# Optimization experiments

Hardware: AMD Instinct MI355X
Metric: run time of the kernel (lower is better)

Reference implementation:

```python
import jax, jax.numpy as jnp
import numpy as np

NUM_TABLES = 10
EMB_DIM = 3
VOCAB = 1_000_000
N_IDX = 4_000_000
N_BAGS = 100_000


def setup_inputs() -> dict:
    key = jax.random.key(0)
    k_idx, k_off, k_w = jax.random.split(key, 3)
    eb_input = jax.random.randint(k_idx, (N_IDX,), 0, VOCAB, dtype=jnp.int64)
    # EmbeddingBag offsets: sorted, first element must be 0, values in [0, N_IDX)
    eb_offset = jnp.sort(jax.random.randint(k_off, (N_BAGS,), 0, N_IDX, dtype=jnp.int64))
    eb_offset = eb_offset.at[0].set(0)
    # torch.nn.EmbeddingBag default init: N(0, 1)
    W = jax.random.normal(k_w, (NUM_TABLES, VOCAB, EMB_DIM), dtype=jnp.float32)
    return {"eb_input": eb_input, "eb_offset": eb_offset, "W": W}


def _bag_sums(eb_input, eb_offset, W):
    # segment id for each index position: bag b covers [offset[b], offset[b+1])
    n = eb_input.shape[0]
    seg = jnp.searchsorted(eb_offset, jnp.arange(n), side="right") - 1  # [N]
    gathered = W[:, eb_input, :]  # [T, N, D] irregular gather
    # sum-pool per bag for every table
    per_bag = jax.vmap(lambda g: jax.ops.segment_sum(g, seg, num_segments=eb_offset.shape[0]))(gathered)  # [T, B, D]
    return per_bag


def reference(eb_input, eb_offset, W):
    per_bag = _bag_sums(eb_input, eb_offset, W)  # [10, B, 3]
    outs = [per_bag[i] for i in range(NUM_TABLES)]
    outs[5] = jnp.sum(outs[5], axis=1, keepdims=True)  # [B, 1]
    outs[6] = jnp.sum(outs[6], axis=1, keepdims=True)  # [B, 1]
    cat = jnp.concatenate(outs, axis=1)  # [B, 26]
    return jnp.sum(cat, axis=0)  # [26]
```

## Files before the change

kernel.cpp:

```cpp
#include <hip/hip_runtime.h>

#define VOCAB 1000000
#define NUM_TABLES 10
#define OUT_SIZE 26
#define BUCKET_BITS 12
#define BPB 4096
#define NBUCKETS 245
#define CHUNK 16384
#define MAXSRC 256
#define GSTRIDE 256
#define RBLOCKS_PER_TABLE 256
#define NRBLK (NUM_TABLES * RBLOCKS_PER_TABLE)
#define RTHREADS 256


__global__ void __launch_bounds__(1024) scatter_kernel(
    const int* __restrict__ idx, int n,
    unsigned short* __restrict__ scat,
    unsigned int* __restrict__ gs32)
{
    __shared__ unsigned int lcount[256];
    __shared__ unsigned int sc[256];
    __shared__ __align__(16) unsigned short stage[CHUNK];
    const int tid = threadIdx.x;
    if (tid < 256) lcount[tid] = 0u;
    __syncthreads();

    const int4* idx4 = (const int4*)idx;
    const int n4 = n >> 2;
    const int base4 = blockIdx.x * (CHUNK / 4);
    int4 q[4];
    bool val[4];
    unsigned rank[16];
    unsigned bkt[16];
#pragma unroll
    for (int j = 0; j < 4; ++j) {
        int i4 = base4 + j * 1024 + tid;
        val[j] = (i4 < n4);
        if (val[j]) q[j] = idx4[i4];
    }
#pragma unroll
    for (int j = 0; j < 4; ++j) {
        if (val[j]) {
            unsigned v[4] = {(unsigned)q[j].x, (unsigned)q[j].y, (unsigned)q[j].z, (unsigned)q[j].w};
#pragma unroll
            for (int e = 0; e < 4; ++e) {
                bkt[j * 4 + e] = v[e] >> BUCKET_BITS;
                rank[j * 4 + e] = atomicAdd(&lcount[bkt[j * 4 + e]], 1u);
            }
        }
    }
    unsigned trank[3], tbkt[3];
    int tcnt = 0;
    if (blockIdx.x == gridDim.x - 1 && tid == 0) {
        for (int i = n4 * 4; i < n; ++i) {
            unsigned u = (unsigned)idx[i];
            tbkt[tcnt] = u >> BUCKET_BITS;
            trank[tcnt] = atomicAdd(&lcount[tbkt[tcnt]], 1u);
            ++tcnt;
        }
    }
    __syncthreads();
    unsigned cnt = 0;
    if (tid < 256) {
        cnt = (tid < NBUCKETS) ? lcount[tid] : 0u;
        sc[tid] = cnt;
    }
    __syncthreads();
#pragma unroll
    for (int off = 1; off < 256; off <<= 1) {
        unsigned v = 0, a = 0;
        if (tid < 256) {
            v = sc[tid];
            if (tid >= off) a = sc[tid - off];
        }
        __syncthreads();
        if (tid < 256) sc[tid] = v + a;
        __syncthreads();
    }
    if (tid < 256) {
        unsigned excl = sc[tid] - cnt;
        if (tid < NBUCKETS) gs32[(size_t)blockIdx.x * GSTRIDE + tid] = excl | (cnt << 16);
        lcount[tid] = excl;
    }
    __syncthreads();
#pragma unroll
    for (int j = 0; j < 4; ++j) {
        if (val[j]) {
            unsigned v[4] = {(unsigned)q[j].x, (unsigned)q[j].y, (unsigned)q[j].z, (unsigned)q[j].w};
#pragma unroll
            for (int e = 0; e < 4; ++e) {
                unsigned k = j * 4 + e;
                stage[lcount[bkt[k]] + rank[k]] = (unsigned short)(v[e] & (BPB - 1));
            }
        }
    }
    if (blockIdx.x == gridDim.x - 1 && tid == 0) {
        for (int i = 0; i < tcnt; ++i) {
            unsigned u = (unsigned)idx[n4 * 4 + i];
            stage[lcount[tbkt[i]] + trank[i]] = (unsigned short)(u & (BPB - 1));
        }
    }
    __syncthreads();
    uint4* dst = (uint4*)(scat + (size_t)blockIdx.x * CHUNK);
    const uint4* src = (const uint4*)stage;
#pragma unroll
    for (int j = 0; j < 2; ++j) dst[j * 1024 + tid] = src[j * 1024 + tid];
}

__global__ void __launch_bounds__(1024) bucket_hist_kernel(
    const unsigned short* __restrict__ scat,
    const unsigned int* __restrict__ gs32, int nsrc,
    unsigned int* __restrict__ hist)
{
    __shared__ __align__(16) unsigned int h[BPB];
    const int b = blockIdx.x;
    const int tid = threadIdx.x;
    const int wave = tid >> 6, lane = tid & 63;
    ((uint4*)h)[tid] = make_uint4(0u, 0u, 0u, 0u);
    __syncthreads();
    for (int s = wave; s < nsrc; s += 16) {
        unsigned g32 = gs32[(size_t)s * GSTRIDE + b];
        unsigned st = g32 & 0xffffu, c = g32 >> 16;
        const unsigned short* p = scat + (size_t)s * CHUNK + st;
        for (unsigned k = lane; k < c; k += 64)
            atomicAdd(&h[p[k]], 1u);
    }
    __syncthreads();
    int nb4 = min(BPB, VOCAB - b * BPB) >> 2;
    uint4* dst = (uint4*)(hist + (size_t)b * BPB);
    const uint4* src = (const uint4*)h;
    if (tid < nb4) dst[tid] = src[tid];
}

__device__ inline float wave_reduce(float v) {
#pragma unroll
    for (int o = 32; o > 0; o >>= 1) v += __shfl_down(v, o, 64);
    return v;
}

__global__ void __launch_bounds__(RTHREADS) reduce_kernel(const float* __restrict__ W,
                                                          const unsigned int* __restrict__ hist,
                                                          float* __restrict__ partials) {
    const int t = blockIdx.x / RBLOCKS_PER_TABLE;
    const int b = blockIdx.x % RBLOCKS_PER_TABLE;
    const float4* __restrict__ W4 = (const float4*)(W + (size_t)t * VOCAB * 3);
    const uint4* __restrict__ h4 = (const uint4*)hist;
    const int ngroups = VOCAB / 4;
    float a0 = 0.f, a1 = 0.f, a2 = 0.f;
    const int stride = RBLOCKS_PER_TABLE * RTHREADS;
    for (int g = b * RTHREADS + (int)threadIdx.x; g < ngroups; g += stride) {
        uint4 c4 = h4[g];
        float4 w0 = W4[3 * g + 0];
        float4 w1 = W4[3 * g + 1];
        float4 w2 = W4[3 * g + 2];
        float c0 = (float)c4.x, c1 = (float)c4.y, c2 = (float)c4.z, c3 = (float)c4.w;
        a0 += c0 * w0.x + c1 * w0.w + c2 * w1.z + c3 * w2.y;
        a1 += c0 * w0.y + c1 * w1.x + c2 * w1.w + c3 * w2.z;
        a2 += c0 * w0.z + c1 * w1.y + c2 * w2.x + c3 * w2.w;
    }
    a0 = wave_reduce(a0);
    a1 = wave_reduce(a1);
    a2 = wave_reduce(a2);
    __shared__ float s[3][4];
    int wave = threadIdx.x >> 6;
    int lane = threadIdx.x & 63;
    if (lane == 0) { s[0][wave] = a0; s[1][wave] = a1; s[2][wave] = a2; }
    __syncthreads();
    if (threadIdx.x == 0) {
        partials[0 * NRBLK + blockIdx.x] = s[0][0] + s[0][1] + s[0][2] + s[0][3];
        partials[1 * NRBLK + blockIdx.x] = s[1][0] + s[1][1] + s[1][2] + s[1][3];
        partials[2 * NRBLK + blockIdx.x] = s[2][0] + s[2][1] + s[2][2] + s[2][3];
    }
}

__global__ void __launch_bounds__(1024) final_kernel(const float* __restrict__ partials,
                                                     float* __restrict__ out) {
    __shared__ float ts[32];
    const int tid = threadIdx.x;
    const int srs = tid >> 5;
    const int j = tid & 31;
    float v = 0.f;
    if (srs < 30) {
        const int t = srs / 3, d = srs % 3;
        const float* p = partials + (size_t)d * NRBLK + t * RBLOCKS_PER_TABLE;
#pragma unroll
        for (int k = 0; k < RBLOCKS_PER_TABLE / 32; ++k) v += p[k * 32 + j];
    }
#pragma unroll
    for (int off = 16; off > 0; off >>= 1) v += __shfl_down(v, off);
    if (j == 0 && srs < 30) ts[srs] = v;
    __syncthreads();
    if (tid < OUT_SIZE) {
        float r;
        if (tid < 15) r = ts[tid];
        else if (tid == 15) r = ts[15] + ts[16] + ts[17];
        else if (tid == 16) r = ts[18] + ts[19] + ts[20];
        else r = ts[tid + 4];
        out[tid] = r;
    }
}


__global__ void zero_kernel_fb(unsigned int* __restrict__ hist, float* __restrict__ out) {
    int i = blockIdx.x * blockDim.x + threadIdx.x;
    int n4 = VOCAB / 4;
    if (i < n4) ((uint4*)hist)[i] = make_uint4(0u, 0u, 0u, 0u);
    if (i < OUT_SIZE) out[i] = 0.0f;
}

__global__ void hist_kernel_fb(const int* __restrict__ idx, unsigned int* __restrict__ hist, int n) {
    int i = blockIdx.x * blockDim.x + threadIdx.x;
    int i4 = i * 4;
    if (i4 + 3 < n) {
        int4 v = ((const int4*)idx)[i];
        atomicAdd(&hist[v.x], 1u);
        atomicAdd(&hist[v.y], 1u);
        atomicAdd(&hist[v.z], 1u);
        atomicAdd(&hist[v.w], 1u);
    } else {
        for (int j = i4; j < n; ++j) atomicAdd(&hist[idx[j]], 1u);
    }
}

__global__ void __launch_bounds__(RTHREADS) reduce_kernel_fb(const float* __restrict__ W,
                                                             const unsigned int* __restrict__ hist,
                                                             float* __restrict__ out) {
    const int t = blockIdx.x / 64;
    const int b = blockIdx.x % 64;
    const float4* __restrict__ W4 = (const float4*)(W + (size_t)t * VOCAB * 3);
    const uint4* __restrict__ h4 = (const uint4*)hist;
    const int ngroups = VOCAB / 4;
    float a0 = 0.f, a1 = 0.f, a2 = 0.f;
    const int stride = 64 * RTHREADS;
    for (int g = b * RTHREADS + (int)threadIdx.x; g < ngroups; g += stride) {
        uint4 c4 = h4[g];
        float4 w0 = W4[3 * g + 0];
        float4 w1 = W4[3 * g + 1];
        float4 w2 = W4[3 * g + 2];
        float c0 = (float)c4.x, c1 = (float)c4.y, c2 = (float)c4.z, c3 = (float)c4.w;
        a0 += c0 * w0.x + c1 * w0.w + c2 * w1.z + c3 * w2.y;
        a1 += c0 * w0.y + c1 * w1.x + c2 * w1.w + c3 * w2.z;
        a2 += c0 * w0.z + c1 * w1.y + c2 * w2.x + c3 * w2.w;
    }
    a0 = wave_reduce(a0);
    a1 = wave_reduce(a1);
    a2 = wave_reduce(a2);
    __shared__ float s[3][4];
    int wave = threadIdx.x >> 6;
    int lane = threadIdx.x & 63;
    if (lane == 0) { s[0][wave] = a0; s[1][wave] = a1; s[2][wave] = a2; }
    __syncthreads();
    if (threadIdx.x == 0) {
        float r0 = s[0][0] + s[0][1] + s[0][2] + s[0][3];
        float r1 = s[1][0] + s[1][1] + s[1][2] + s[1][3];
        float r2 = s[2][0] + s[2][1] + s[2][2] + s[2][3];
        if (t == 5) atomicAdd(&out[15], r0 + r1 + r2);
        else if (t == 6) atomicAdd(&out[16], r0 + r1 + r2);
        else {
            int base = (t < 5) ? t * 3 : 17 + (t - 7) * 3;
            atomicAdd(&out[base + 0], r0);
            atomicAdd(&out[base + 1], r1);
            atomicAdd(&out[base + 2], r2);
        }
    }
}


extern "C" void kernel_launch(void* const* d_in, const int* in_sizes, int n_in,
                              void* d_out, int out_size, void* d_ws, size_t ws_size,
                              hipStream_t stream) {
    const int* eb_input = (const int*)d_in[0];
    const float* W = (const float*)d_in[2];
    float* out = (float*)d_out;
    int n_idx = in_sizes[0];

    const int nsrc = (n_idx + CHUNK - 1) / CHUNK;
    const size_t scat_bytes = (size_t)MAXSRC * CHUNK * 2;
    const size_t gs_off = scat_bytes;
    const size_t gs_bytes = (size_t)MAXSRC * GSTRIDE * 4;
    const size_t hist_off = gs_off + gs_bytes;
    const size_t hist_bytes = (size_t)VOCAB * 4;
    const size_t part_off = (hist_off + hist_bytes + 255) & ~(size_t)255;
    const size_t need = part_off + (size_t)3 * NRBLK * 4;

    if (nsrc <= MAXSRC && ws_size >= need) {
        unsigned short* scat = (unsigned short*)d_ws;
        unsigned int* gs32 = (unsigned int*)((char*)d_ws + gs_off);
        unsigned int* hist = (unsigned int*)((char*)d_ws + hist_off);
        float* partials = (float*)((char*)d_ws + part_off);

        scatter_kernel<<<nsrc, 1024, 0, stream>>>(eb_input, n_idx, scat, gs32);
        bucket_hist_kernel<<<NBUCKETS, 1024, 0, stream>>>(scat, gs32, nsrc, hist);
        reduce_kernel<<<NRBLK, RTHREADS, 0, stream>>>(W, hist, partials);
        final_kernel<<<1, 1024, 0, stream>>>(partials, out);
    } else {
        unsigned int* hist = (unsigned int*)d_ws;
        int zblocks = (VOCAB / 4 + 255) / 256;
        zero_kernel_fb<<<zblocks, 256, 0, stream>>>(hist, out);
        int hthreads = (n_idx + 3) / 4;
        int hblocks = (hthreads + 255) / 256;
        hist_kernel_fb<<<hblocks, 256, 0, stream>>>(eb_input, hist, n_idx);
        reduce_kernel_fb<<<NUM_TABLES * 64, RTHREADS, 0, stream>>>(W, hist, out);
    }
}
```

Before: 207.7 us.

## Fuse final reduction into reduce kernel via last-block counter; load hist once across tables

Result: slower. 466.5 us (+124.6%).

```diff
diff --git a/kernel.cpp b/kernel.cpp
--- a/kernel.cpp
+++ b/kernel.cpp
@@ -9,20 +9,23 @@
 #define CHUNK 16384
 #define MAXSRC 256
 #define GSTRIDE 256
-#define RBLOCKS_PER_TABLE 256
-#define NRBLK (NUM_TABLES * RBLOCKS_PER_TABLE)
-#define RTHREADS 256
+#define NGROUPS (VOCAB / 4)
+#define RBLK ((NGROUPS + 255) / 256)
+#define NPW (RBLK * 4)
+#define NSERIES 30
 
 
 __global__ void __launch_bounds__(1024) scatter_kernel(
     const int* __restrict__ idx, int n,
     unsigned short* __restrict__ scat,
-    unsigned int* __restrict__ gs32)
+    unsigned int* __restrict__ gs32,
+    unsigned int* __restrict__ counter)
 {
     __shared__ unsigned int lcount[256];
     __shared__ unsigned int sc[256];
     __shared__ __align__(16) unsigned short stage[CHUNK];
     const int tid = threadIdx.x;
+    if (blockIdx.x == 0 && tid == 0) *counter = 0u;
     if (tid < 256) lcount[tid] = 0u;
     __syncthreads();
 
@@ -114,13 +117,15 @@
     unsigned int* __restrict__ hist)
 {
     __shared__ __align__(16) unsigned int h[BPB];
+    __shared__ unsigned int gcol[MAXSRC];
     const int b = blockIdx.x;
     const int tid = threadIdx.x;
+    ((uint4*)h)[tid] = make_uint4(0u, 0u, 0u, 0u);
+    if (tid < nsrc) gcol[tid] = gs32[(size_t)tid * GSTRIDE + b];
+    __syncthreads();
     const int wave = tid >> 6, lane = tid & 63;
-    ((uint4*)h)[tid] = make_uint4(0u, 0u, 0u, 0u);
-    __syncthreads();
     for (int s = wave; s < nsrc; s += 16) {
-        unsigned g32 = gs32[(size_t)s * GSTRIDE + b];
+        unsigned g32 = gcol[s];
         unsigned st = g32 & 0xffffu, c = g32 >> 16;
         const unsigned short* p = scat + (size_t)s * CHUNK + st;
         for (unsigned k = lane; k < c; k += 64)
@@ -139,64 +144,66 @@
     return v;
 }
 
-__global__ void __launch_bounds__(RTHREADS) reduce_kernel(const float* __restrict__ W,
-                                                          const unsigned int* __restrict__ hist,
-                                                          float* __restrict__ partials) {
-    const int t = blockIdx.x / RBLOCKS_PER_TABLE;
-    const int b = blockIdx.x % RBLOCKS_PER_TABLE;
-    const float4* __restrict__ W4 = (const float4*)(W + (size_t)t * VOCAB * 3);
-    const uint4* __restrict__ h4 = (const uint4*)hist;
-    const int ngroups = VOCAB / 4;
-    float a0 = 0.f, a1 = 0.f, a2 = 0.f;
-    const int stride = RBLOCKS_PER_TABLE * RTHREADS;
-    for (int g = b * RTHREADS + (int)threadIdx.x; g < ngroups; g += stride) {
-        uint4 c4 = h4[g];
-        float4 w0 = W4[3 * g + 0];
-        float4 w1 = W4[3 * g + 1];
-        float4 w2 = W4[3 * g + 2];
-        float c0 = (float)c4.x, c1 = (float)c4.y, c2 = (float)c4.z, c3 = (float)c4.w;
-        a0 += c0 * w0.x + c1 * w0.w + c2 * w1.z + c3 * w2.y;
-        a1 += c0 * w0.y + c1 * w1.x + c2 * w1.w + c3 * w2.z;
-        a2 += c0 * w0.z + c1 * w1.y + c2 * w2.x + c3 * w2.w;
-    }
-    a0 = wave_reduce(a0);
-    a1 = wave_reduce(a1);
-    a2 = wave_reduce(a2);
-    __shared__ float s[3][4];
-    int wave = threadIdx.x >> 6;
-    int lane = threadIdx.x & 63;
-    if (lane == 0) { s[0][wave] = a0; s[1][wave] = a1; s[2][wave] = a2; }
-    __syncthreads();
-    if (threadIdx.x == 0) {
-        partials[0 * NRBLK + blockIdx.x] = s[0][0] + s[0][1] + s[0][2] + s[0][3];
-        partials[1 * NRBLK + blockIdx.x] = s[1][0] + s[1][1] + s[1][2] + s[1][3];
-        partials[2 * NRBLK + blockIdx.x] = s[2][0] + s[2][1] + s[2][2] + s[2][3];
-    }
-}
-
-__global__ void __launch_bounds__(1024) final_kernel(const float* __restrict__ partials,
-                                                     float* __restrict__ out) {
-    __shared__ float ts[32];
+__global__ void __launch_bounds__(256) reduce_kernel(
+    const float* __restrict__ W,
+    const unsigned int* __restrict__ hist,
+    float* __restrict__ partials,
+    unsigned int* __restrict__ counter,
+    float* __restrict__ out)
+{
     const int tid = threadIdx.x;
-    const int srs = tid >> 5;
-    const int j = tid & 31;
+    const int g = blockIdx.x * 256 + tid;
+    const int wave = tid >> 6, lane = tid & 63;
+    const bool act = (g < NGROUPS);
+    uint4 c4 = make_uint4(0u, 0u, 0u, 0u);
+    if (act) c4 = ((const uint4*)hist)[g];
+    const float c0 = (float)c4.x, c1 = (float)c4.y, c2 = (float)c4.z, c3 = (float)c4.w;
+    const int pb = blockIdx.x * 4 + wave;
+#pragma unroll 2
+    for (int t = 0; t < NUM_TABLES; ++t) {
+        float a0 = 0.f, a1 = 0.f, a2 = 0.f;
+        if (act) {
+            const float4* __restrict__ W4 = (const float4*)(W + (size_t)t * VOCAB * 3);
+            float4 w0 = W4[3 * g + 0];
+            float4 w1 = W4[3 * g + 1];
+            float4 w2 = W4[3 * g + 2];
+            a0 = c0 * w0.x + c1 * w0.w + c2 * w1.z + c3 * w2.y;
+            a1 = c0 * w0.y + c1 * w1.x + c2 * w1.w + c3 * w2.z;
+            a2 = c0 * w0.z + c1 * w1.y + c2 * w2.x + c3 * w2.w;
+        }
+        a0 = wave_reduce(a0);
+        a1 = wave_reduce(a1);
+        a2 = wave_reduce(a2);
+        if (lane == 0) {
+            partials[(size_t)(t * 3 + 0) * NPW + pb] = a0;
+            partials[(size_t)(t * 3 + 1) * NPW + pb] = a1;
+            partials[(size_t)(t * 3 + 2) * NPW + pb] = a2;
+        }
+    }
+    __threadfence();
+    __shared__ unsigned int done;
+    if (tid == 0) done = atomicAdd(counter, 1u);
+    __syncthreads();
+    if (done != (unsigned)gridDim.x - 1u) return;
+    __threadfence();
+
+    __shared__ float smf[32];
+    const int srs = tid >> 3, j = tid & 7;
     float v = 0.f;
-    if (srs < 30) {
-        const int t = srs / 3, d = srs % 3;
-        const float* p = partials + (size_t)d * NRBLK + t * RBLOCKS_PER_TABLE;
-#pragma unroll
-        for (int k = 0; k < RBLOCKS_PER_TABLE / 32; ++k) v += p[k * 32 + j];
-    }
-#pragma unroll
-    for (int off = 16; off > 0; off >>= 1) v += __shfl_down(v, off);
-    if (j == 0 && srs < 30) ts[srs] = v;
+    if (srs < NSERIES) {
+        const float* p = partials + (size_t)srs * NPW;
+        for (int i = j; i < NPW; i += 8) v += p[i];
+    }
+#pragma unroll
+    for (int off = 4; off > 0; off >>= 1) v += __shfl_down(v, off, 8);
+    if (srs < NSERIES && j == 0) smf[srs] = v;
     __syncthreads();
     if (tid < OUT_SIZE) {
         float r;
-        if (tid < 15) r = ts[tid];
-        else if (tid == 15) r = ts[15] + ts[16] + ts[17];
-        else if (tid == 16) r = ts[18] + ts[19] + ts[20];
-        else r = ts[tid + 4];
+        if (tid < 15) r = smf[tid];
+        else if (tid == 15) r = smf[15] + smf[16] + smf[17];
+        else if (tid == 16) r = smf[18] + smf[19] + smf[20];
+        else r = smf[tid + 4];
         out[tid] = r;
     }
 }
@@ -223,17 +230,17 @@
     }
 }
 
-__global__ void __launch_bounds__(RTHREADS) reduce_kernel_fb(const float* __restrict__ W,
-                                                             const unsigned int* __restrict__ hist,
-                                                             float* __restrict__ out) {
+__global__ void __launch_bounds__(256) reduce_kernel_fb(const float* __restrict__ W,
+                                                        const unsigned int* __restrict__ hist,
+                                                        float* __restrict__ out) {
     const int t = blockIdx.x / 64;
     const int b = blockIdx.x % 64;
     const float4* __restrict__ W4 = (const float4*)(W + (size_t)t * VOCAB * 3);
     const uint4* __restrict__ h4 = (const uint4*)hist;
     const int ngroups = VOCAB / 4;
     float a0 = 0.f, a1 = 0.f, a2 = 0.f;
-    const int stride = 64 * RTHREADS;
-    for (int g = b * RTHREADS + (int)threadIdx.x; g < ngroups; g += stride) {
+    const int stride = 64 * 256;
+    for (int g = b * 256 + (int)threadIdx.x; g < ngroups; g += stride) {
         uint4 c4 = h4[g];
         float4 w0 = W4[3 * g + 0];
         float4 w1 = W4[3 * g + 1];
@@ -282,18 +289,20 @@
     const size_t hist_off = gs_off + gs_bytes;
     const size_t hist_bytes = (size_t)VOCAB * 4;
     const size_t part_off = (hist_off + hist_bytes + 255) & ~(size_t)255;
-    const size_t need = part_off + (size_t)3 * NRBLK * 4;
+    const size_t part_bytes = (size_t)NSERIES * NPW * 4;
+    const size_t cnt_off = (part_off + part_bytes + 255) & ~(size_t)255;
+    const size_t need = cnt_off + 256;
 
     if (nsrc <= MAXSRC && ws_size >= need) {
         unsigned short* scat = (unsigned short*)d_ws;
         unsigned int* gs32 = (unsigned int*)((char*)d_ws + gs_off);
         unsigned int* hist = (unsigned int*)((char*)d_ws + hist_off);
         float* partials = (float*)((char*)d_ws + part_off);
-
-        scatter_kernel<<<nsrc, 1024, 0, stream>>>(eb_input, n_idx, scat, gs32);
+        unsigned int* counter = (unsigned int*)((char*)d_ws + cnt_off);
+
+        scatter_kernel<<<nsrc, 1024, 0, stream>>>(eb_input, n_idx, scat, gs32, counter);
         bucket_hist_kernel<<<NBUCKETS, 1024, 0, stream>>>(scat, gs32, nsrc, hist);
-        reduce_kernel<<<NRBLK, RTHREADS, 0, stream>>>(W, hist, partials);
-        final_kernel<<<1, 1024, 0, stream>>>(partials, out);
+        reduce_kernel<<<RBLK, 256, 0, stream>>>(W, hist, partials, counter, out);
     } else {
         unsigned int* hist = (unsigned int*)d_ws;
         int zblocks = (VOCAB / 4 + 255) / 256;
@@ -301,6 +310,6 @@
         int hthreads = (n_idx + 3) / 4;
         int hblocks = (hthreads + 255) / 256;
         hist_kernel_fb<<<hblocks, 256, 0, stream>>>(eb_input, hist, n_idx);
-        reduce_kernel_fb<<<NUM_TABLES * 64, RTHREADS, 0, stream>>>(W, hist, out);
-    }
-}
+        reduce_kernel_fb<<<NUM_TABLES * 64, 256, 0, stream>>>(W, hist, out);
+    }
+}
```
